# Performance work log

Measured on AMD Instinct MI355X. Metric: run time of the kernel, lower is better.

The kernel has to match this reference:

```python
import jax, jax.numpy as jnp
import numpy as np

SEQ_LEN = 4096
D_IN = 1024
D_OUT = 1024


def setup_inputs() -> dict:
    key = jax.random.key(0)
    k_x, k_q, k_k, k_v = jax.random.split(key, 4)
    s = 1.0 / np.sqrt(D_IN)
    return {
        "x": jax.random.normal(k_x, (SEQ_LEN, D_IN), dtype=jnp.float32),
        "W_query": jax.random.normal(k_q, (D_IN, D_OUT), dtype=jnp.float32) * s,
        "W_key": jax.random.normal(k_k, (D_IN, D_OUT), dtype=jnp.float32) * s,
        "W_value": jax.random.normal(k_v, (D_IN, D_OUT), dtype=jnp.float32) * s,
    }


def reference(x, W_query, W_key, W_value):
    # QKV projections (Linear without bias): [S, d_out]
    q = x @ W_query
    k = x @ W_key
    v = x @ W_value
    # Full S x S score matrix, causal mask, scaled softmax
    scores = q @ k.T  # [S, S]
    seq_len = x.shape[0]
    causal = jnp.tril(jnp.ones((seq_len, seq_len), dtype=bool))
    scores = jnp.where(causal, scores, -jnp.inf)
    scale = 1.0 / jnp.sqrt(jnp.asarray(k.shape[-1], dtype=scores.dtype))
    attn = jax.nn.softmax(scores * scale, axis=-1)
    return attn @ v  # [S, d_out]
```

## Files before the change

### kernel.cpp

```cpp
#include <hip/hip_runtime.h>
#include <math.h>

#define SEQ 4096
#define DIM 1024

typedef unsigned short u16;
typedef __attribute__((ext_vector_type(8))) short short8;
typedef __attribute__((ext_vector_type(4))) float floatx4;
typedef __attribute__((ext_vector_type(4))) unsigned short us4;

__device__ __forceinline__ float bf2f(u16 u) {
    union { unsigned int i; float f; } c; c.i = ((unsigned int)u) << 16; return c.f;
}
__device__ __forceinline__ u16 f2bf(float f) {
    union { float f; unsigned int i; } c; c.f = f;
    return (u16)((c.i + 0x7fffu + ((c.i >> 16) & 1u)) >> 16);
}
__device__ __forceinline__ void gload_lds16(const u16* g, u16* l) {
    __builtin_amdgcn_global_load_lds((const __attribute__((address_space(1))) void*)g,
                                     (__attribute__((address_space(3))) void*)l, 16, 0, 0);
}

template <int MODE>
__global__ __launch_bounds__(256) void gemm_nt(const u16* __restrict__ A,
                                               const u16* __restrict__ B,
                                               void* __restrict__ Cv,
                                               float* __restrict__ Ppart,
                                               int lda, int ldb, int ldc, int Kdim,
                                               float scale0, float scale1) {
    const int row0 = blockIdx.y * 128;
    const int col0 = blockIdx.x * 128;
    if (MODE == 1 && col0 > row0) return;
    int kbeg = 0, kend = Kdim, chunk = 0;
    if (MODE == 2) {
        chunk = blockIdx.z;
        kbeg = chunk << 10;
        const int klim = row0 + 128;
        if (kbeg >= klim) return;
        kend = min(kbeg + 1024, klim);
    }

    __shared__ u16 As[2][4096];
    __shared__ u16 Bs[2][4096];

    const int tid  = threadIdx.x;
    const int wave = tid >> 6;
    const int lane = tid & 63;
    const int wm = wave & 1;
    const int wn = wave >> 1;

    const int ch0 = wave * 128 + lane;
    const int ch1 = ch0 + 64;
    const u16* aP0 = A + (size_t)(row0 + (ch0 >> 2)) * lda + kbeg + (ch0 & 3) * 8;
    const u16* aP1 = A + (size_t)(row0 + (ch1 >> 2)) * lda + kbeg + (ch1 & 3) * 8;
    const u16* bP0 = B + (size_t)(col0 + (ch0 >> 2)) * ldb + kbeg + (ch0 & 3) * 8;
    const u16* bP1 = B + (size_t)(col0 + (ch1 >> 2)) * ldb + kbeg + (ch1 & 3) * 8;
    const int l0 = wave * 1024;

    floatx4 acc[4][4] = {};
    const int niter = (kend - kbeg) >> 5;
    const int frow = lane & 15;
    const int fk   = (lane >> 4) * 8;

    gload_lds16(aP0, &As[0][l0]);
    gload_lds16(aP1, &As[0][l0 + 512]);
    gload_lds16(bP0, &Bs[0][l0]);
    gload_lds16(bP1, &Bs[0][l0 + 512]);
    aP0 += 32; aP1 += 32; bP0 += 32; bP1 += 32;

    for (int it = 0; it < niter; ++it) {
        const int cur = it & 1;
        __syncthreads();
        if (it + 1 < niter) {
            const int nxt = cur ^ 1;
            gload_lds16(aP0, &As[nxt][l0]);
            gload_lds16(aP1, &As[nxt][l0 + 512]);
            gload_lds16(bP0, &Bs[nxt][l0]);
            gload_lds16(bP1, &Bs[nxt][l0 + 512]);
            aP0 += 32; aP1 += 32; bP0 += 32; bP1 += 32;
        }
        __builtin_amdgcn_sched_barrier(0);
        short8 af[4], bfr[4];
#pragma unroll
        for (int t = 0; t < 4; ++t) {
            af[t]  = *(const short8*)&As[cur][(wm * 64 + t * 16 + frow) * 32 + fk];
            bfr[t] = *(const short8*)&Bs[cur][(wn * 64 + t * 16 + frow) * 32 + fk];
        }
#pragma unroll
        for (int mt = 0; mt < 4; ++mt)
#pragma unroll
            for (int nt = 0; nt < 4; ++nt)
                acc[mt][nt] = __builtin_amdgcn_mfma_f32_16x16x32_bf16(
                    af[mt], bfr[nt], acc[mt][nt], 0, 0, 0);
    }

    const int cr = (lane >> 4) * 4;
    const int cc = lane & 15;
    if (MODE == 2) {
        float* dst;
        if (chunk == 0) {
            dst = (float*)Cv;
        } else {
            const ptrdiff_t poff[3] = {0, (ptrdiff_t)3072 * 1024, (ptrdiff_t)5120 * 1024};
            dst = Ppart + poff[chunk - 1] - (ptrdiff_t)(chunk << 10) * 1024;
        }
#pragma unroll
        for (int mt = 0; mt < 4; ++mt)
#pragma unroll
            for (int nt = 0; nt < 4; ++nt)
#pragma unroll
                for (int r = 0; r < 4; ++r) {
                    const int row = row0 + wm * 64 + mt * 16 + cr + r;
                    const int col = col0 + wn * 64 + nt * 16 + cc;
                    dst[(size_t)row * ldc + col] = acc[mt][nt][r];
                }
    } else {
        u16* dst = (u16*)Cv;
        const float sc = (col0 < 1024) ? scale0 : scale1;
#pragma unroll
        for (int mt = 0; mt < 4; ++mt)
#pragma unroll
            for (int nt = 0; nt < 4; ++nt)
#pragma unroll
                for (int r = 0; r < 4; ++r) {
                    const int row = row0 + wm * 64 + mt * 16 + cr + r;
                    const int col = col0 + wn * 64 + nt * 16 + cc;
                    dst[(size_t)row * ldc + col] = f2bf(acc[mt][nt][r] * sc);
                }
    }
}

__global__ __launch_bounds__(256) void transpose_cast(const float* __restrict__ W0,
                                                      const float* __restrict__ W1,
                                                      const float* __restrict__ W2,
                                                      u16* __restrict__ Wt) {
    __shared__ float tile[32][33];
    const float* W = (blockIdx.z == 0) ? W0 : (blockIdx.z == 1) ? W1 : W2;
    u16* out = Wt + (size_t)blockIdx.z * DIM * DIM;
    const int bx = blockIdx.x * 32;
    const int by = blockIdx.y * 32;
    const int tx = threadIdx.x & 31;
    const int ty = (threadIdx.x >> 5) * 4;
#pragma unroll
    for (int r = 0; r < 4; ++r)
        tile[ty + r][tx] = W[(size_t)(by + ty + r) * DIM + bx + tx];
    __syncthreads();
#pragma unroll
    for (int r = 0; r < 4; ++r)
        out[(size_t)(bx + ty + r) * DIM + by + tx] = f2bf(tile[tx][ty + r]);
}

__global__ __launch_bounds__(256) void cast_bf16(const float* __restrict__ X,
                                                 u16* __restrict__ Xb) {
    const size_t i = ((size_t)blockIdx.x * 256 + threadIdx.x) * 4;
    const float4 v = *(const float4*)(X + i);
    us4 o = { f2bf(v.x), f2bf(v.y), f2bf(v.z), f2bf(v.w) };
    *(us4*)(Xb + i) = o;
}

__global__ __launch_bounds__(256) void transpose_v(const u16* __restrict__ QKV,
                                                   u16* __restrict__ Vt) {
    __shared__ u16 t[64][68];
    const int vc0 = blockIdx.x * 64;
    const int vr0 = blockIdx.y * 64;
    const int tid = threadIdx.x;
    const int tx4 = (tid & 15) * 4;
    const int r0 = tid >> 4;
#pragma unroll
    for (int p = 0; p < 4; ++p) {
        const int r = r0 + p * 16;
        *(us4*)&t[r][tx4] = *(const us4*)&QKV[(size_t)(vr0 + r) * 3072 + 2048 + vc0 + tx4];
    }
    __syncthreads();
#pragma unroll
    for (int p = 0; p < 4; ++p) {
        const int c = r0 + p * 16;
        us4 o = { t[tx4 + 0][c], t[tx4 + 1][c], t[tx4 + 2][c], t[tx4 + 3][c] };
        *(us4*)&Vt[(size_t)(vc0 + c) * SEQ + vr0 + tx4] = o;
    }
}

__global__ __launch_bounds__(256) void softmax_causal_bf16(u16* __restrict__ S) {
    __shared__ float red[4];
    __shared__ float bc;
    const int i = blockIdx.x;
    u16* row = S + (size_t)i * SEQ;
    const int n = i + 1;
    const int tid = threadIdx.x;
    const int zend = (i & ~127) + 128;

    float v[16];
    float m = -3.4e38f;
#pragma unroll
    for (int t = 0; t < 16; ++t) {
        const int j = tid + (t << 8);
        if (j < n) { v[t] = bf2f(row[j]); m = fmaxf(m, v[t]); }
    }
#pragma unroll
    for (int o = 32; o > 0; o >>= 1) m = fmaxf(m, __shfl_down(m, o));
    if ((tid & 63) == 0) red[tid >> 6] = m;
    __syncthreads();
    if (tid == 0) bc = fmaxf(fmaxf(red[0], red[1]), fmaxf(red[2], red[3]));
    __syncthreads();
    m = bc;

    float s = 0.f;
#pragma unroll
    for (int t = 0; t < 16; ++t) {
        const int j = tid + (t << 8);
        if (j < n) { v[t] = __expf(v[t] - m); s += v[t]; }
    }
#pragma unroll
    for (int o = 32; o > 0; o >>= 1) s += __shfl_down(s, o);
    if ((tid & 63) == 0) red[tid >> 6] = s;
    __syncthreads();
    if (tid == 0) bc = 1.0f / (red[0] + red[1] + red[2] + red[3]);
    __syncthreads();
    const float inv = bc;

#pragma unroll
    for (int t = 0; t < 16; ++t) {
        const int j = tid + (t << 8);
        if (j < n) row[j] = f2bf(v[t] * inv);
        else if (j < zend) row[j] = 0;
    }
}

__global__ __launch_bounds__(256) void reduce_pv(float* __restrict__ O,
                                                 const float* __restrict__ P) {
    const int r = blockIdx.x;
    const int row = 1024 + r;
    const int col = threadIdx.x * 4;
    float4 a = *(const float4*)(O + (size_t)row * 1024 + col);
    const float4 b1 = *(const float4*)(P + (size_t)r * 1024 + col);
    a.x += b1.x; a.y += b1.y; a.z += b1.z; a.w += b1.w;
    if (row >= 2048) {
        const float4 b2 = *(const float4*)(P + (size_t)3072 * 1024 +
                                           (size_t)(row - 2048) * 1024 + col);
        a.x += b2.x; a.y += b2.y; a.z += b2.z; a.w += b2.w;
    }
    if (row >= 3072) {
        const float4 b3 = *(const float4*)(P + (size_t)5120 * 1024 +
                                           (size_t)(row - 3072) * 1024 + col);
        a.x += b3.x; a.y += b3.y; a.z += b3.z; a.w += b3.w;
    }
    *(float4*)(O + (size_t)row * 1024 + col) = a;
}

extern "C" void kernel_launch(void* const* d_in, const int* in_sizes, int n_in,
                              void* d_out, int out_size, void* d_ws, size_t ws_size,
                              hipStream_t stream) {
    const float* x  = (const float*)d_in[0];
    const float* Wq = (const float*)d_in[1];
    const float* Wk = (const float*)d_in[2];
    const float* Wv = (const float*)d_in[3];

    u16* xb    = (u16*)d_ws;
    u16* Wt    = xb  + (size_t)SEQ * DIM;
    u16* QKV   = Wt  + (size_t)3072 * DIM;
    u16* Vt    = QKV + (size_t)SEQ * 3072;
    u16* S     = Vt  + (size_t)DIM * SEQ;
    float* Ppart = (float*)(S + (size_t)SEQ * SEQ);

    cast_bf16<<<SEQ * DIM / 1024, 256, 0, stream>>>(x, xb);
    transpose_cast<<<dim3(32, 32, 3), 256, 0, stream>>>(Wq, Wk, Wv, Wt);

    gemm_nt<0><<<dim3(24, 32), 256, 0, stream>>>(
        xb, Wt, QKV, nullptr, DIM, DIM, 3072, DIM, 0.03125f, 1.0f);

    transpose_v<<<dim3(16, 64), 256, 0, stream>>>(QKV, Vt);

    gemm_nt<1><<<dim3(32, 32), 256, 0, stream>>>(
        QKV, QKV + 1024, S, nullptr, 3072, 3072, SEQ, DIM, 1.0f, 1.0f);

    softmax_causal_bf16<<<SEQ, 256, 0, stream>>>(S);

    gemm_nt<2><<<dim3(8, 32, 4), 256, 0, stream>>>(
        S, Vt, d_out, Ppart, SEQ, SEQ, DIM, SEQ, 1.0f, 1.0f);

    reduce_pv<<<3072, 256, 0, stream>>>((float*)d_out, Ppart);
}
```

Baseline: 232.8 us.

## Swizzle GEMM LDS layout and write V transposed from projection epilogue

The GEMM tiles now use an XOR swizzle on the 16-byte k-chunks in LDS, applied both when the global-to-LDS loads pick their source chunk and when fragments are read, to reduce LDS bank conflicts on the short8 fragment reads. The QKV projection epilogue writes the V columns directly in transposed form into Vt with 4-element vector stores, which removes the separate transpose_v kernel and its extra round trip through memory. The QK buffer shrinks to 2048 columns. The transposed stores are strided by SEQ, which may coalesce less well than row-major stores.

```diff
diff --git a/kernel.cpp b/kernel.cpp
--- a/kernel.cpp
+++ b/kernel.cpp
@@ -26,8 +26,9 @@
                                                const u16* __restrict__ B,
                                                void* __restrict__ Cv,
                                                float* __restrict__ Ppart,
+                                               u16* __restrict__ VtOut,
                                                int lda, int ldb, int ldc, int Kdim,
-                                               float scale0, float scale1) {
+                                               float scale0) {
     const int row0 = blockIdx.y * 128;
     const int col0 = blockIdx.x * 128;
     if (MODE == 1 && col0 > row0) return;
@@ -49,18 +50,20 @@
     const int wm = wave & 1;
     const int wn = wave >> 1;
 
-    const int ch0 = wave * 128 + lane;
-    const int ch1 = ch0 + 64;
-    const u16* aP0 = A + (size_t)(row0 + (ch0 >> 2)) * lda + kbeg + (ch0 & 3) * 8;
-    const u16* aP1 = A + (size_t)(row0 + (ch1 >> 2)) * lda + kbeg + (ch1 & 3) * 8;
-    const u16* bP0 = B + (size_t)(col0 + (ch0 >> 2)) * ldb + kbeg + (ch0 & 3) * 8;
-    const u16* bP1 = B + (size_t)(col0 + (ch1 >> 2)) * ldb + kbeg + (ch1 & 3) * 8;
+    const int s0 = wave * 128 + lane;
+    const int s1 = s0 + 64;
+    const int r0s = s0 >> 2, q0s = ((s0 & 3) ^ ((s0 >> 3) & 3)) * 8;
+    const int r1s = s1 >> 2, q1s = ((s1 & 3) ^ ((s1 >> 3) & 3)) * 8;
+    const u16* aP0 = A + (size_t)(row0 + r0s) * lda + kbeg + q0s;
+    const u16* aP1 = A + (size_t)(row0 + r1s) * lda + kbeg + q1s;
+    const u16* bP0 = B + (size_t)(col0 + r0s) * ldb + kbeg + q0s;
+    const u16* bP1 = B + (size_t)(col0 + r1s) * ldb + kbeg + q1s;
     const int l0 = wave * 1024;
 
     floatx4 acc[4][4] = {};
     const int niter = (kend - kbeg) >> 5;
     const int frow = lane & 15;
-    const int fk   = (lane >> 4) * 8;
+    const int xq = (((lane >> 4) ^ ((frow >> 1) & 3))) * 8;
 
     gload_lds16(aP0, &As[0][l0]);
     gload_lds16(aP1, &As[0][l0 + 512]);
@@ -83,8 +86,8 @@
         short8 af[4], bfr[4];
 #pragma unroll
         for (int t = 0; t < 4; ++t) {
-            af[t]  = *(const short8*)&As[cur][(wm * 64 + t * 16 + frow) * 32 + fk];
-            bfr[t] = *(const short8*)&Bs[cur][(wn * 64 + t * 16 + frow) * 32 + fk];
+            af[t]  = *(const short8*)&As[cur][(wm * 64 + t * 16 + frow) * 32 + xq];
+            bfr[t] = *(const short8*)&Bs[cur][(wn * 64 + t * 16 + frow) * 32 + xq];
         }
 #pragma unroll
         for (int mt = 0; mt < 4; ++mt)
@@ -114,9 +117,20 @@
                     const int col = col0 + wn * 64 + nt * 16 + cc;
                     dst[(size_t)row * ldc + col] = acc[mt][nt][r];
                 }
+    } else if (MODE == 0 && col0 >= 2048) {
+#pragma unroll
+        for (int mt = 0; mt < 4; ++mt)
+#pragma unroll
+            for (int nt = 0; nt < 4; ++nt) {
+                const int row = row0 + wm * 64 + mt * 16 + cr;
+                const int col = (col0 - 2048) + wn * 64 + nt * 16 + cc;
+                us4 o = { f2bf(acc[mt][nt][0]), f2bf(acc[mt][nt][1]),
+                          f2bf(acc[mt][nt][2]), f2bf(acc[mt][nt][3]) };
+                *(us4*)&VtOut[(size_t)col * SEQ + row] = o;
+            }
     } else {
         u16* dst = (u16*)Cv;
-        const float sc = (col0 < 1024) ? scale0 : scale1;
+        const float sc = (MODE == 0 && col0 < 1024) ? scale0 : 1.0f;
 #pragma unroll
         for (int mt = 0; mt < 4; ++mt)
 #pragma unroll
@@ -156,28 +170,6 @@
     const float4 v = *(const float4*)(X + i);
     us4 o = { f2bf(v.x), f2bf(v.y), f2bf(v.z), f2bf(v.w) };
     *(us4*)(Xb + i) = o;
-}
-
-__global__ __launch_bounds__(256) void transpose_v(const u16* __restrict__ QKV,
-                                                   u16* __restrict__ Vt) {
-    __shared__ u16 t[64][68];
-    const int vc0 = blockIdx.x * 64;
-    const int vr0 = blockIdx.y * 64;
-    const int tid = threadIdx.x;
-    const int tx4 = (tid & 15) * 4;
-    const int r0 = tid >> 4;
-#pragma unroll
-    for (int p = 0; p < 4; ++p) {
-        const int r = r0 + p * 16;
-        *(us4*)&t[r][tx4] = *(const us4*)&QKV[(size_t)(vr0 + r) * 3072 + 2048 + vc0 + tx4];
-    }
-    __syncthreads();
-#pragma unroll
-    for (int p = 0; p < 4; ++p) {
-        const int c = r0 + p * 16;
-        us4 o = { t[tx4 + 0][c], t[tx4 + 1][c], t[tx4 + 2][c], t[tx4 + 3][c] };
-        *(us4*)&Vt[(size_t)(vc0 + c) * SEQ + vr0 + tx4] = o;
-    }
 }
 
 __global__ __launch_bounds__(256) void softmax_causal_bf16(u16* __restrict__ S) {
@@ -257,8 +249,8 @@
 
     u16* xb    = (u16*)d_ws;
     u16* Wt    = xb  + (size_t)SEQ * DIM;
-    u16* QKV   = Wt  + (size_t)3072 * DIM;
-    u16* Vt    = QKV + (size_t)SEQ * 3072;
+    u16* QK    = Wt  + (size_t)3072 * DIM;
+    u16* Vt    = QK  + (size_t)SEQ * 2048;
     u16* S     = Vt  + (size_t)DIM * SEQ;
     float* Ppart = (float*)(S + (size_t)SEQ * SEQ);
 
@@ -266,17 +258,15 @@
     transpose_cast<<<dim3(32, 32, 3), 256, 0, stream>>>(Wq, Wk, Wv, Wt);
 
     gemm_nt<0><<<dim3(24, 32), 256, 0, stream>>>(
-        xb, Wt, QKV, nullptr, DIM, DIM, 3072, DIM, 0.03125f, 1.0f);
-
-    transpose_v<<<dim3(16, 64), 256, 0, stream>>>(QKV, Vt);
+        xb, Wt, QK, nullptr, Vt, DIM, DIM, 2048, DIM, 0.03125f);
 
     gemm_nt<1><<<dim3(32, 32), 256, 0, stream>>>(
-        QKV, QKV + 1024, S, nullptr, 3072, 3072, SEQ, DIM, 1.0f, 1.0f);
+        QK, QK + 1024, S, nullptr, nullptr, 2048, 2048, SEQ, DIM, 1.0f);
 
     softmax_causal_bf16<<<SEQ, 256, 0, stream>>>(S);
 
     gemm_nt<2><<<dim3(8, 32, 4), 256, 0, stream>>>(
-        S, Vt, d_out, Ppart, SEQ, SEQ, DIM, SEQ, 1.0f, 1.0f);
+        S, Vt, d_out, Ppart, nullptr, SEQ, SEQ, DIM, SEQ, 1.0f);
 
     reduce_pv<<<3072, 256, 0, stream>>>((float*)d_out, Ppart);
 }
```

Result: faster. 224.6 us (-3.5%).
